# Kernel optimization log

Hardware: AMD Instinct MI355X
Metric: run time of the kernel (lower is better)

The kernel has to match this reference:

```python
import jax, jax.numpy as jnp
import numpy as np

MARGIN = 0.1
N = 16384


def setup_inputs() -> dict:
    key = jax.random.key(0)
    k1, k2 = jax.random.split(key)
    pred = jax.random.normal(k1, (N,), dtype=jnp.float32)
    target = jax.random.uniform(k2, (N,), dtype=jnp.float32)
    return {"pred": pred, "target": target}


def reference(pred, target):
    # mask[i, j] = target[j] < target[i]  (the Python loop's Tj per row i)
    mask = target[None, :] < target[:, None]            # [N, N] bool
    # hinge[i, j] = max(0, margin - (pred[i] - pred[j]))
    hinge = jnp.maximum(0.0, MARGIN - (pred[:, None] - pred[None, :]))
    row_sum = jnp.sum(jnp.where(mask, hinge, 0.0), axis=1)   # [N]
    cnt = jnp.sum(mask, axis=1)                               # [N] int
    # rows with no j such that target[j] < target[i] are skipped (continue)
    per_row = jnp.where(cnt > 0, row_sum / jnp.maximum(cnt, 1).astype(pred.dtype), 0.0)
    return jnp.sum(per_row) / pred.shape[0]
```

## Files before the change

### kernel.cpp

```cpp
#include <hip/hip_runtime.h>


constexpr float MARGIN = 0.1f;
constexpr int R = 8;
constexpr int T = 256;

__global__ __launch_bounds__(T) void rank_rows(const float* __restrict__ pred,
                                               const float* __restrict__ target,
                                               float* __restrict__ out,
                                               int n, float inv_n) {
    const int base = blockIdx.x * R;

    float ti[R], ci[R];
    #pragma unroll
    for (int r = 0; r < R; ++r) {
        ti[r] = target[base + r];
        ci[r] = MARGIN - pred[base + r];
    }

    float sum[R];
    unsigned int cnt[R];
    #pragma unroll
    for (int r = 0; r < R; ++r) { sum[r] = 0.f; cnt[r] = 0u; }

    const float4* __restrict__ t4 = (const float4*)target;
    const float4* __restrict__ p4 = (const float4*)pred;
    const int n4 = n >> 2;

    #pragma unroll 4
    for (int j = (int)threadIdx.x; j < n4; j += T) {
        const float4 tj = t4[j];
        const float4 pj = p4[j];
        #pragma unroll
        for (int r = 0; r < R; ++r) {
            const float tir = ti[r], cir = ci[r];
            {
                const bool m = tj.x < tir;
                const float h = fmaxf(0.f, cir + pj.x);
                sum[r] += m ? h : 0.f;
                cnt[r] += (unsigned)__popcll(__ballot(m));
            }
            {
                const bool m = tj.y < tir;
                const float h = fmaxf(0.f, cir + pj.y);
                sum[r] += m ? h : 0.f;
                cnt[r] += (unsigned)__popcll(__ballot(m));
            }
            {
                const bool m = tj.z < tir;
                const float h = fmaxf(0.f, cir + pj.z);
                sum[r] += m ? h : 0.f;
                cnt[r] += (unsigned)__popcll(__ballot(m));
            }
            {
                const bool m = tj.w < tir;
                const float h = fmaxf(0.f, cir + pj.w);
                sum[r] += m ? h : 0.f;
                cnt[r] += (unsigned)__popcll(__ballot(m));
            }
        }
    }

    __shared__ float        ls[T / 64][R];
    __shared__ unsigned int lc[T / 64][R];
    __shared__ float        row_val[R];
    const int lane = threadIdx.x & 63;
    const int wv   = threadIdx.x >> 6;

    #pragma unroll
    for (int r = 0; r < R; ++r) {
        float s = sum[r];
        #pragma unroll
        for (int off = 32; off > 0; off >>= 1) s += __shfl_down(s, off, 64);
        if (lane == 0) { ls[wv][r] = s; lc[wv][r] = cnt[r]; }
    }
    __syncthreads();

    if ((int)threadIdx.x < R) {
        float s = 0.f;
        unsigned int c = 0u;
        #pragma unroll
        for (int w = 0; w < T / 64; ++w) { s += ls[w][threadIdx.x]; c += lc[w][threadIdx.x]; }
        row_val[threadIdx.x] = (c > 0u) ? (s / (float)c) : 0.f;
    }
    __syncthreads();

    if (threadIdx.x == 0) {
        float local = 0.f;
        #pragma unroll
        for (int r = 0; r < R; ++r) local += row_val[r];
        atomicAdd(out, local * inv_n);
    }
}

extern "C" void kernel_launch(void* const* d_in, const int* in_sizes, int n_in,
                              void* d_out, int out_size, void* d_ws, size_t ws_size,
                              hipStream_t stream) {
    const float* pred   = (const float*)d_in[0];
    const float* target = (const float*)d_in[1];
    const int n = in_sizes[0];

    float* out = (float*)d_out;
    hipMemsetAsync(out, 0, sizeof(float) * (size_t)out_size, stream);

    rank_rows<<<n / R, T, 0, stream>>>(pred, target, out, n, 1.0f / (float)n);
}
```

Before: 96.89 us.

## Rank rows by target, scatter into sorted order, sum hinge over prefix only

Splits the work into two kernels. The first counts, for each row, how many targets are strictly smaller (its rank) and scatters pred and that count into rank-sorted order, using an atomic tie counter. The second sums the hinge only over the sorted prefix, which removes the mask compare and select from the main loop and halves the average number of elements visited. It adds a second launch, a workspace memset, atomic scatter traffic, and relies on tied targets sharing the same prefix.

Measured after the change: 112.0 us. 15.6% more time.

```diff
diff --git a/kernel.cpp b/kernel.cpp
--- a/kernel.cpp
+++ b/kernel.cpp
@@ -2,93 +2,126 @@
 
 
 constexpr float MARGIN = 0.1f;
-constexpr int R = 8;
-constexpr int T = 256;
+constexpr int T   = 256;
+constexpr int R1  = 16;
+constexpr int R2  = 8;
 
-__global__ __launch_bounds__(T) void rank_rows(const float* __restrict__ pred,
-                                               const float* __restrict__ target,
-                                               float* __restrict__ out,
-                                               int n, float inv_n) {
-    const int base = blockIdx.x * R;
+__global__ __launch_bounds__(T) void rank_scatter(const float* __restrict__ pred,
+                                                  const float* __restrict__ target,
+                                                  float* __restrict__ p_sorted,
+                                                  int* __restrict__ K_sorted,
+                                                  unsigned int* __restrict__ tie_ctr,
+                                                  int n) {
+    const int base = blockIdx.x * R1;
 
-    float ti[R], ci[R];
+    float ti[R1];
     #pragma unroll
-    for (int r = 0; r < R; ++r) {
-        ti[r] = target[base + r];
-        ci[r] = MARGIN - pred[base + r];
-    }
+    for (int r = 0; r < R1; ++r) ti[r] = target[base + r];
 
-    float sum[R];
-    unsigned int cnt[R];
+    unsigned int cnt[R1];
     #pragma unroll
-    for (int r = 0; r < R; ++r) { sum[r] = 0.f; cnt[r] = 0u; }
+    for (int r = 0; r < R1; ++r) cnt[r] = 0u;
 
     const float4* __restrict__ t4 = (const float4*)target;
-    const float4* __restrict__ p4 = (const float4*)pred;
     const int n4 = n >> 2;
 
-    #pragma unroll 4
     for (int j = (int)threadIdx.x; j < n4; j += T) {
         const float4 tj = t4[j];
-        const float4 pj = p4[j];
         #pragma unroll
-        for (int r = 0; r < R; ++r) {
-            const float tir = ti[r], cir = ci[r];
-            {
-                const bool m = tj.x < tir;
-                const float h = fmaxf(0.f, cir + pj.x);
-                sum[r] += m ? h : 0.f;
-                cnt[r] += (unsigned)__popcll(__ballot(m));
-            }
-            {
-                const bool m = tj.y < tir;
-                const float h = fmaxf(0.f, cir + pj.y);
-                sum[r] += m ? h : 0.f;
-                cnt[r] += (unsigned)__popcll(__ballot(m));
-            }
-            {
-                const bool m = tj.z < tir;
-                const float h = fmaxf(0.f, cir + pj.z);
-                sum[r] += m ? h : 0.f;
-                cnt[r] += (unsigned)__popcll(__ballot(m));
-            }
-            {
-                const bool m = tj.w < tir;
-                const float h = fmaxf(0.f, cir + pj.w);
-                sum[r] += m ? h : 0.f;
-                cnt[r] += (unsigned)__popcll(__ballot(m));
-            }
+        for (int r = 0; r < R1; ++r) {
+            const float tir = ti[r];
+            cnt[r] += (unsigned)__popcll(__ballot(tj.x < tir));
+            cnt[r] += (unsigned)__popcll(__ballot(tj.y < tir));
+            cnt[r] += (unsigned)__popcll(__ballot(tj.z < tir));
+            cnt[r] += (unsigned)__popcll(__ballot(tj.w < tir));
         }
     }
 
-    __shared__ float        ls[T / 64][R];
-    __shared__ unsigned int lc[T / 64][R];
-    __shared__ float        row_val[R];
+    __shared__ unsigned int lc[T / 64][R1];
+    const int lane = threadIdx.x & 63;
+    const int wv   = threadIdx.x >> 6;
+    if (lane == 0) {
+        #pragma unroll
+        for (int r = 0; r < R1; ++r) lc[wv][r] = cnt[r];
+    }
+    __syncthreads();
+
+    if ((int)threadIdx.x < R1) {
+        const int r = threadIdx.x;
+        const unsigned int strict = lc[0][r] + lc[1][r] + lc[2][r] + lc[3][r];
+        const int slot = (int)strict + (int)atomicAdd(&tie_ctr[strict], 1u);
+        p_sorted[slot] = pred[base + r];
+        K_sorted[slot] = (int)strict;
+    }
+}
+
+__global__ __launch_bounds__(T) void hinge_sorted(const float* __restrict__ p_sorted,
+                                                  const int* __restrict__ K_sorted,
+                                                  float* __restrict__ out,
+                                                  int n, float inv_n) {
+    const int base = blockIdx.x * R2;
+
+    float c[R2];
+    int   K[R2];
+    #pragma unroll
+    for (int r = 0; r < R2; ++r) {
+        K[r] = K_sorted[base + r];
+        c[r] = MARGIN - p_sorted[base + r];
+    }
+    const int Kmin = K[0];
+    const int Kmax = K[R2 - 1];
+
+    float sum[R2];
+    #pragma unroll
+    for (int r = 0; r < R2; ++r) sum[r] = 0.f;
+
+    const float4* __restrict__ p4 = (const float4*)p_sorted;
+    const int n4m = Kmin >> 2;
+    for (int j = (int)threadIdx.x; j < n4m; j += T) {
+        const float4 p = p4[j];
+        #pragma unroll
+        for (int r = 0; r < R2; ++r) {
+            const float cr = c[r];
+            sum[r] += fmaxf(0.f, cr + p.x);
+            sum[r] += fmaxf(0.f, cr + p.y);
+            sum[r] += fmaxf(0.f, cr + p.z);
+            sum[r] += fmaxf(0.f, cr + p.w);
+        }
+    }
+
+    for (int j = (n4m << 2) + (int)threadIdx.x; j < Kmax; j += T) {
+        const float pj = p_sorted[j];
+        #pragma unroll
+        for (int r = 0; r < R2; ++r) {
+            sum[r] += (j < K[r]) ? fmaxf(0.f, c[r] + pj) : 0.f;
+        }
+    }
+
+    __shared__ float ls[T / 64][R2];
+    __shared__ float row_val[R2];
     const int lane = threadIdx.x & 63;
     const int wv   = threadIdx.x >> 6;
 
     #pragma unroll
-    for (int r = 0; r < R; ++r) {
+    for (int r = 0; r < R2; ++r) {
         float s = sum[r];
         #pragma unroll
         for (int off = 32; off > 0; off >>= 1) s += __shfl_down(s, off, 64);
-        if (lane == 0) { ls[wv][r] = s; lc[wv][r] = cnt[r]; }
+        if (lane == 0) ls[wv][r] = s;
     }
     __syncthreads();
 
-    if ((int)threadIdx.x < R) {
-        float s = 0.f;
-        unsigned int c = 0u;
-        #pragma unroll
-        for (int w = 0; w < T / 64; ++w) { s += ls[w][threadIdx.x]; c += lc[w][threadIdx.x]; }
-        row_val[threadIdx.x] = (c > 0u) ? (s / (float)c) : 0.f;
+    if ((int)threadIdx.x < R2) {
+        const int r = threadIdx.x;
+        const float s = ls[0][r] + ls[1][r] + ls[2][r] + ls[3][r];
+        row_val[r] = (K[r] > 0) ? (s / (float)K[r]) : 0.f;
     }
     __syncthreads();
 
     if (threadIdx.x == 0) {
         float local = 0.f;
         #pragma unroll
-        for (int r = 0; r < R; ++r) local += row_val[r];
+        for (int r = 0; r < R2; ++r) local += row_val[r];
         atomicAdd(out, local * inv_n);
     }
 }
@@ -100,8 +133,14 @@
     const float* target = (const float*)d_in[1];
     const int n = in_sizes[0];
 
+    float*        p_sorted = (float*)d_ws;
+    int*          K_sorted = (int*)((char*)d_ws + (size_t)n * 4);
+    unsigned int* tie_ctr  = (unsigned int*)((char*)d_ws + (size_t)n * 8);
+
     float* out = (float*)d_out;
     hipMemsetAsync(out, 0, sizeof(float) * (size_t)out_size, stream);
+    hipMemsetAsync(tie_ctr, 0, (size_t)n * 4, stream);
 
-    rank_rows<<<n / R, T, 0, stream>>>(pred, target, out, n, 1.0f / (float)n);
+    rank_scatter<<<n / R1, T, 0, stream>>>(pred, target, p_sorted, K_sorted, tie_ctr, n);
+    hinge_sorted<<<n / R2, T, 0, stream>>>(p_sorted, K_sorted, out, n, 1.0f / (float)n);
 }
```
